# Kernel optimization log

Hardware: AMD Instinct MI355X
Metric: run time of the kernel (lower is better)

The kernel has to match this reference:

```python
import jax, jax.numpy as jnp
import numpy as np

D_MODEL = 1024
NUM_HEADS = 16
DEPTH = D_MODEL // NUM_HEADS
B, S = 2, 2048


def setup_inputs() -> dict:
    key = jax.random.key(0)
    ks = jax.random.split(key, 12)
    s = 1.0 / np.sqrt(D_MODEL)
    return {
        "query": jax.random.normal(ks[0], (B, S, D_MODEL), jnp.float32),
        "key": jax.random.normal(ks[1], (B, S, D_MODEL), jnp.float32),
        "value": jax.random.normal(ks[2], (B, S, D_MODEL), jnp.float32),
        "mask": jax.random.randint(ks[3], (B, S), 0, 2, jnp.int32),
        "Wq": jax.random.normal(ks[4], (D_MODEL, D_MODEL), jnp.float32) * s,
        "bq": jnp.zeros((D_MODEL,), jnp.float32),
        "Wk": jax.random.normal(ks[5], (D_MODEL, D_MODEL), jnp.float32) * s,
        "bk": jnp.zeros((D_MODEL,), jnp.float32),
        "Wv": jax.random.normal(ks[6], (D_MODEL, D_MODEL), jnp.float32) * s,
        "bv": jnp.zeros((D_MODEL,), jnp.float32),
        "Wo": jax.random.normal(ks[7], (D_MODEL, D_MODEL), jnp.float32) * s,
        "bo": jnp.zeros((D_MODEL,), jnp.float32),
    }


def _split_heads(x):
    # [B, S, D] -> [B, H, S, depth]
    b, s, _ = x.shape
    return x.reshape(b, s, NUM_HEADS, DEPTH).transpose(0, 2, 1, 3)


def reference(query, key, value, mask, Wq, bq, Wk, bk, Wv, bv, Wo, bo):
    q = _split_heads(query @ Wq.T + bq)
    k = _split_heads(key @ Wk.T + bk)
    v = _split_heads(value @ Wv.T + bv)
    scale = 1.0 / jnp.sqrt(jnp.float32(DEPTH))
    # [B, H, Sq, Sk]
    logits = jnp.einsum("bhqd,bhkd->bhqk", q, k) * scale
    logits = logits + mask.astype(logits.dtype)[:, None, None, :] * (-1e9)
    attn = jax.nn.softmax(logits, axis=-1)
    out = jnp.einsum("bhqk,bhkd->bhqd", attn, v)
    out = out.transpose(0, 2, 1, 3).reshape(query.shape[0], -1, D_MODEL)
    return out @ Wo.T + bo
```

## Files before the change

### kernel.cpp

```cpp
#include <hip/hip_runtime.h>

typedef _Float16 half8 __attribute__((ext_vector_type(8)));
typedef _Float16 half4 __attribute__((ext_vector_type(4)));
typedef __fp16  fp16x2 __attribute__((ext_vector_type(2)));
typedef float floatx4 __attribute__((ext_vector_type(4)));

#define D_MODEL 1024
#define NHEAD   16
#define DH      64
#define BATCH   2
#define SEQ     2048
#define M_TOT   4096
#define NT      (SEQ / 128)

#define SCALE_L2E 0.18033688011112042f
#define MASK_L2E  (-1.4426950408889634e9f)

#define GLD_LDS16(g, l)                                                          \
  __builtin_amdgcn_global_load_lds(                                              \
      (const __attribute__((address_space(1))) void*)(g),                        \
      (__attribute__((address_space(3))) void*)(l), 16, 0, 0)

__device__ inline half4 pk4(floatx4 v) {
  union { fp16x2 h2[2]; half4 h4; } u;
  u.h2[0] = __builtin_amdgcn_cvt_pkrtz(v[0], v[1]);
  u.h2[1] = __builtin_amdgcn_cvt_pkrtz(v[2], v[3]);
  return u.h4;
}

__global__ __launch_bounds__(256) void cvt_all(const float* __restrict__ q,
                                               const float* __restrict__ k,
                                               const float* __restrict__ v,
                                               const float* __restrict__ wq,
                                               const float* __restrict__ wk,
                                               const float* __restrict__ wv,
                                               const float* __restrict__ wo,
                                               _Float16* __restrict__ Xall,
                                               _Float16* __restrict__ Wall) {
  int bid = blockIdx.x;
  const float* src;
  _Float16* dst;
  if (bid < 6144) {
    int tsr = bid >> 11;
    src = (tsr == 0) ? q : (tsr == 1) ? k : v;
    dst = Xall + (size_t)tsr * 4194304;
    bid &= 2047;
  } else {
    int w = (bid - 6144) >> 9;
    src = (w == 0) ? wq : (w == 1) ? wk : (w == 2) ? wv : wo;
    dst = Wall + (size_t)w * 1048576;
    bid = (bid - 6144) & 511;
  }
  int off = bid * 2048 + threadIdx.x * 8;
  float4 a = *(const float4*)(src + off);
  float4 b = *(const float4*)(src + off + 4);
  half8 h;
  h[0] = (_Float16)a.x; h[1] = (_Float16)a.y; h[2] = (_Float16)a.z; h[3] = (_Float16)a.w;
  h[4] = (_Float16)b.x; h[5] = (_Float16)b.y; h[6] = (_Float16)b.z; h[7] = (_Float16)b.w;
  *(half8*)(dst + off) = h;
}

__global__ __launch_bounds__(256) void gemm_qkv(const _Float16* __restrict__ Xall,
                                                const _Float16* __restrict__ Wall,
                                                const float* __restrict__ bq,
                                                const float* __restrict__ bk,
                                                const float* __restrict__ bv,
                                                _Float16* __restrict__ Obase) {
  __shared__ alignas(16) char smem[32768];
  _Float16 (*As)[64]  = (_Float16(*)[64])smem;
  _Float16 (*Bs)[64]  = (_Float16(*)[64])(smem + 16384);
  _Float16 (*Ts)[136] = (_Float16(*)[136])smem;

  const int bid = blockIdx.x;
  const int xcd = bid & 7;
  const int g = bid >> 3;
  const int p = xcd * 12 + (g >> 3);
  const int z = p >> 5;
  const int m0 = (p & 31) * 128;
  const int n0 = (g & 7) * 128;

  const _Float16* X = Xall + (size_t)z * 4194304;
  const _Float16* W = Wall + (size_t)z * 1048576;
  const float* bias = (z == 0) ? bq : (z == 1) ? bk : bv;
  _Float16* out = Obase + (size_t)z * 4194304;

  const int t = threadIdx.x, lane = t & 63, wave = t >> 6;
  const int wr = wave >> 1, wc = wave & 1;
  const int fr = lane & 15, quad = lane >> 4, rg = quad * 4;
  const int fsw = fr & 7;

  floatx4 acc[4][4];
  for (int i = 0; i < 4; i++)
    for (int j = 0; j < 4; j++) acc[i][j] = (floatx4){0.f, 0.f, 0.f, 0.f};

  const int rl = lane >> 3, pc = lane & 7;
  const int gcol = ((pc ^ rl) * 8);
  const _Float16* gA[4];
  const _Float16* gB[4];
  _Float16* lA[4];
  _Float16* lB[4];
  for (int i = 0; i < 4; i++) {
    int row = wave * 32 + i * 8 + rl;
    gA[i] = X + (size_t)(m0 + row) * 1024 + gcol;
    gB[i] = W + (size_t)(n0 + row) * 1024 + gcol;
    lA[i] = &As[wave * 32 + i * 8][0];
    lB[i] = &Bs[wave * 32 + i * 8][0];
  }

  for (int k0 = 0; k0 < 1024; k0 += 64) {
    for (int i = 0; i < 4; i++) GLD_LDS16(gA[i] + k0, lA[i]);
    for (int i = 0; i < 4; i++) GLD_LDS16(gB[i] + k0, lB[i]);
    __syncthreads();

    for (int kk = 0; kk < 2; kk++) {
      const int csw = (((kk << 2) | quad) ^ fsw) * 8;
      half8 af[4], bw[4];
      for (int i = 0; i < 4; i++) {
        af[i] = *(const half8*)&As[wr * 64 + i * 16 + fr][csw];
        bw[i] = *(const half8*)&Bs[wc * 64 + i * 16 + fr][csw];
      }
      for (int i = 0; i < 4; i++)
        for (int j = 0; j < 4; j++)
          acc[i][j] = __builtin_amdgcn_mfma_f32_16x16x32_f16(af[i], bw[j], acc[i][j], 0, 0, 0);
    }
    __syncthreads();
  }

  if (z != 2) {
    for (int i = 0; i < 4; i++)
      for (int j = 0; j < 4; j++) {
        int n = n0 + wc * 64 + j * 16 + fr;
        float bv2 = bias[n];
        int hh = n >> 6, d = n & 63;
        for (int r = 0; r < 4; r++) {
          int m = m0 + wr * 64 + i * 16 + rg + r;
          int bb = m >> 11, s = m & 2047;
          out[(((size_t)(bb * NHEAD + hh)) * SEQ + s) * DH + d] =
              (_Float16)(acc[i][j][r] + bv2);
        }
      }
  } else {
    const int bb = m0 >> 11, s0 = m0 & 2047;
    for (int p2 = 0; p2 < 2; p2++) {
      __syncthreads();
      if (wc == p2) {
        for (int j = 0; j < 4; j++) {
          float bv2 = bias[n0 + p2 * 64 + j * 16 + fr];
          for (int i = 0; i < 4; i++)
            for (int r = 0; r < 4; r++)
              Ts[j * 16 + fr][wr * 64 + i * 16 + rg + r] =
                  (_Float16)(acc[i][j][r] + bv2);
        }
      }
      __syncthreads();
      int dd = t >> 2, c4 = (t & 3) * 32;
      int hh = (n0 >> 6) + p2;
      _Float16* dst = out + (((size_t)(bb * NHEAD + hh)) * DH + dd) * SEQ + s0;
      for (int u = 0; u < 4; u++)
        *(half8*)(dst + c4 + u * 8) = *(const half8*)&Ts[dd][c4 + u * 8];
    }
  }
}

__global__ __launch_bounds__(256) void gemm_wo(const _Float16* __restrict__ ctx,
                                               const _Float16* __restrict__ W,
                                               const float* __restrict__ bias,
                                               float* __restrict__ out) {
  __shared__ alignas(16) _Float16 As[128][64];
  __shared__ alignas(16) _Float16 Bs[128][64];

  const int t = threadIdx.x, lane = t & 63, wave = t >> 6;
  const int wr = wave >> 1, wc = wave & 1;
  const int m0 = blockIdx.y * 128, n0 = blockIdx.x * 128;
  const int fr = lane & 15, quad = lane >> 4, rg = quad * 4;
  const int fsw = fr & 7;

  floatx4 acc[4][4];
  for (int i = 0; i < 4; i++)
    for (int j = 0; j < 4; j++) acc[i][j] = (floatx4){0.f, 0.f, 0.f, 0.f};

  const int rl = lane >> 3, pc = lane & 7;
  const int gcol = ((pc ^ rl) * 8);
  const _Float16* gA[4];
  const _Float16* gB[4];
  _Float16* lA[4];
  _Float16* lB[4];
  for (int i = 0; i < 4; i++) {
    int row = wave * 32 + i * 8 + rl;
    gA[i] = ctx + (size_t)(m0 + row) * 1024 + gcol;
    gB[i] = W + (size_t)(n0 + row) * 1024 + gcol;
    lA[i] = &As[wave * 32 + i * 8][0];
    lB[i] = &Bs[wave * 32 + i * 8][0];
  }

  for (int k0 = 0; k0 < 1024; k0 += 64) {
    for (int i = 0; i < 4; i++) GLD_LDS16(gA[i] + k0, lA[i]);
    for (int i = 0; i < 4; i++) GLD_LDS16(gB[i] + k0, lB[i]);
    __syncthreads();

    for (int kk = 0; kk < 2; kk++) {
      const int csw = (((kk << 2) | quad) ^ fsw) * 8;
      half8 af[4], bw[4];
      for (int i = 0; i < 4; i++) {
        af[i] = *(const half8*)&As[wr * 64 + i * 16 + fr][csw];
        bw[i] = *(const half8*)&Bs[wc * 64 + i * 16 + fr][csw];
      }
      for (int i = 0; i < 4; i++)
        for (int j = 0; j < 4; j++)
          acc[i][j] = __builtin_amdgcn_mfma_f32_16x16x32_f16(af[i], bw[j], acc[i][j], 0, 0, 0);
    }
    __syncthreads();
  }

  for (int i = 0; i < 4; i++)
    for (int j = 0; j < 4; j++) {
      int n = n0 + wc * 64 + j * 16 + fr;
      float bv2 = bias[n];
      for (int r = 0; r < 4; r++) {
        int m = m0 + wr * 64 + i * 16 + rg + r;
        out[(size_t)m * D_MODEL + n] = acc[i][j][r] + bv2;
      }
    }
}

__global__ __launch_bounds__(256) void attn_kernel(const _Float16* __restrict__ Qp,
                                                   const _Float16* __restrict__ Kp,
                                                   const _Float16* __restrict__ VT,
                                                   const int* __restrict__ mask,
                                                   _Float16* __restrict__ ctx) {
  __shared__ alignas(16) _Float16 Ks[128][64];
  __shared__ alignas(16) _Float16 Vt[64][128];
  __shared__ float Msf[128];

  const int bid = blockIdx.x;
  const int hh = bid & 31;
  const int q0 = (bid >> 5) * 128;
  const int b = hh >> 4, h = hh & 15;

  const int t = threadIdx.x, lane = t & 63, wave = t >> 6;
  const int fr = lane & 15, quad = lane >> 4, fc = quad * 8;
  const int fsw = fr & 7;

  const _Float16* Kg  = Kp + (size_t)hh * SEQ * DH;
  const _Float16* VTg = VT + (size_t)hh * DH * SEQ;

  const _Float16* kG[4];
  {
    const int kr = lane >> 3, kp = lane & 7;
    for (int i = 0; i < 4; i++) {
      int krow = wave * 32 + i * 8 + kr;
      kG[i] = Kg + (size_t)krow * DH + ((kp ^ kr) * 8);
    }
  }

  const int svr = t >> 2;
  const int svc = (t & 3) * 4;

  half8 qf[2][2];
  {
    const _Float16* Qgw = Qp + ((size_t)hh * SEQ + q0 + wave * 32) * DH;
    for (int mi = 0; mi < 2; mi++)
      for (int kk = 0; kk < 2; kk++)
        qf[mi][kk] = *(const half8*)(Qgw + (mi * 16 + fr) * DH + kk * 32 + fc);
  }

  float lr[2][2] = {{0.f, 0.f}, {0.f, 0.f}};
  floatx4 oaccT[4][2];
  for (int dj = 0; dj < 4; dj++)
    for (int mi = 0; mi < 2; mi++) oaccT[dj][mi] = (floatx4){0.f, 0.f, 0.f, 0.f};

  for (int kt = 0; kt < NT; kt++) {
    const int k0 = kt * 128;

    for (int i = 0; i < 4; i++)
      GLD_LDS16(kG[i] + (size_t)k0 * DH, &Ks[wave * 32 + i * 8][0]);

    {
      const half8* gv = (const half8*)(VTg + (size_t)svr * SEQ + k0);
      half8 vb[4];
      for (int u = 0; u < 4; u++) vb[u] = gv[svc + u];
      const int rsw = svr & 7;
      for (int u = 0; u < 4; u++) {
        const int g = svc + u;
        const int t8p = g >> 2, par = (g >> 1) & 1, qA = (g & 1) * 2;
        const int v4lo = t8p * 8 + qA * 2 + par;
        const int v4hi = v4lo + 2;
        union { half8 h8; half4 h4[2]; } uv; uv.h8 = vb[u];
        *(half4*)&Vt[svr][((v4lo >> 1) ^ rsw) * 8 + (v4lo & 1) * 4] = uv.h4[0];
        *(half4*)&Vt[svr][((v4hi >> 1) ^ rsw) * 8 + (v4hi & 1) * 4] = uv.h4[1];
      }
    }
    if (t < 128) Msf[t] = (float)mask[b * SEQ + k0 + t] * MASK_L2E;
    __syncthreads();

    floatx4 saT[8][2];
#pragma unroll
    for (int t8 = 0; t8 < 8; t8++) {
      saT[t8][0] = (floatx4){0.f, 0.f, 0.f, 0.f};
      saT[t8][1] = (floatx4){0.f, 0.f, 0.f, 0.f};
      half8 kf0 = *(const half8*)&Ks[t8 * 16 + fr][(quad ^ fsw) * 8];
      half8 kf1 = *(const half8*)&Ks[t8 * 16 + fr][((4 | quad) ^ fsw) * 8];
      saT[t8][0] = __builtin_amdgcn_mfma_f32_16x16x32_f16(kf0, qf[0][0], saT[t8][0], 0, 0, 0);
      saT[t8][1] = __builtin_amdgcn_mfma_f32_16x16x32_f16(kf0, qf[1][0], saT[t8][1], 0, 0, 0);
      saT[t8][0] = __builtin_amdgcn_mfma_f32_16x16x32_f16(kf1, qf[0][1], saT[t8][0], 0, 0, 0);
      saT[t8][1] = __builtin_amdgcn_mfma_f32_16x16x32_f16(kf1, qf[1][1], saT[t8][1], 0, 0, 0);
    }

    floatx4 mk[8];
#pragma unroll
    for (int t8 = 0; t8 < 8; t8++)
      mk[t8] = *(const floatx4*)&Msf[t8 * 16 + quad * 4];

#pragma unroll
    for (int mi = 0; mi < 2; mi++) {
      float rs0 = 0.f, rs1 = 0.f;
#pragma unroll
      for (int t8 = 0; t8 < 8; t8++) {
        floatx4 p;
#pragma unroll
        for (int r = 0; r < 4; r++)
          p[r] = __builtin_amdgcn_exp2f(saT[t8][mi][r] * SCALE_L2E + mk[t8][r]);
        saT[t8][mi] = p;
        if (t8 & 1) rs1 += (p[0] + p[1]) + (p[2] + p[3]);
        else        rs0 += (p[0] + p[1]) + (p[2] + p[3]);
      }
      lr[mi][0] += rs0;
      lr[mi][1] += rs1;
    }

#pragma unroll
    for (int t8p = 0; t8p < 4; t8p++) {
      half4 pb0a = pk4(saT[2 * t8p][0]);
      half4 pb0b = pk4(saT[2 * t8p][1]);
      half4 pb1a = pk4(saT[2 * t8p + 1][0]);
      half4 pb1b = pk4(saT[2 * t8p + 1][1]);
      const int c = t8p * 4 + quad;
#pragma unroll
      for (int dj = 0; dj < 4; dj++) {
        const int d = dj * 16 + fr;
        union { half8 h8; half4 h4[2]; } uv;
        uv.h8 = *(const half8*)&Vt[d][(c ^ (d & 7)) * 8];
        oaccT[dj][0] = __builtin_amdgcn_mfma_f32_16x16x16f16(uv.h4[0], pb0a, oaccT[dj][0], 0, 0, 0);
        oaccT[dj][1] = __builtin_amdgcn_mfma_f32_16x16x16f16(uv.h4[0], pb0b, oaccT[dj][1], 0, 0, 0);
        oaccT[dj][0] = __builtin_amdgcn_mfma_f32_16x16x16f16(uv.h4[1], pb1a, oaccT[dj][0], 0, 0, 0);
        oaccT[dj][1] = __builtin_amdgcn_mfma_f32_16x16x16f16(uv.h4[1], pb1b, oaccT[dj][1], 0, 0, 0);
      }
    }
    __syncthreads();
  }

#pragma unroll
  for (int mi = 0; mi < 2; mi++) {
    float l = lr[mi][0] + lr[mi][1];
    l += __shfl_xor(l, 16);
    l += __shfl_xor(l, 32);
    float inv = 1.0f / l;
    int qrow = q0 + wave * 32 + mi * 16 + fr;
    _Float16* o = ctx + ((size_t)b * SEQ + qrow) * D_MODEL + h * DH;
#pragma unroll
    for (int dj = 0; dj < 4; dj++) {
      half4 st;
      for (int r = 0; r < 4; r++) st[r] = (_Float16)(oaccT[dj][mi][r] * inv);
      *(half4*)(o + dj * 16 + quad * 4) = st;
    }
  }
}

extern "C" void kernel_launch(void* const* d_in, const int* in_sizes, int n_in,
                              void* d_out, int out_size, void* d_ws, size_t ws_size,
                              hipStream_t stream) {
  const float* query = (const float*)d_in[0];
  const float* key   = (const float*)d_in[1];
  const float* value = (const float*)d_in[2];
  const int*   mask  = (const int*)d_in[3];
  const float* Wq = (const float*)d_in[4];
  const float* bq = (const float*)d_in[5];
  const float* Wk = (const float*)d_in[6];
  const float* bk = (const float*)d_in[7];
  const float* Wv = (const float*)d_in[8];
  const float* bv = (const float*)d_in[9];
  const float* Wo = (const float*)d_in[10];
  const float* bo = (const float*)d_in[11];

  char* ws = (char*)d_ws;
  _Float16* Xall = (_Float16*)(ws);
  _Float16* Wall = (_Float16*)(ws + (size_t)24 * 1024 * 1024);
  _Float16* Qp   = (_Float16*)(ws + (size_t)32 * 1024 * 1024);
  _Float16* ctx  = (_Float16*)(ws + (size_t)56 * 1024 * 1024);

  _Float16* Kp = Qp + (size_t)4194304;
  _Float16* VT = Qp + (size_t)8388608;

  cvt_all<<<8192, 256, 0, stream>>>(query, key, value, Wq, Wk, Wv, Wo, Xall, Wall);

  gemm_qkv<<<dim3(768), 256, 0, stream>>>(Xall, Wall, bq, bk, bv, Qp);

  attn_kernel<<<dim3(512), 256, 0, stream>>>(Qp, Kp, VT, mask, ctx);

  gemm_wo<<<dim3(8, 32), 256, 0, stream>>>(ctx, Wall + (size_t)3 * 1048576, bo, (float*)d_out);
}
```

Before: 238.8 us.

## Fuse fp32-to-fp16 activation conversion into the QKV projection GEMM

```diff
diff --git a/kernel.cpp b/kernel.cpp
--- a/kernel.cpp
+++ b/kernel.cpp
@@ -28,29 +28,16 @@
   return u.h4;
 }
 
-__global__ __launch_bounds__(256) void cvt_all(const float* __restrict__ q,
-                                               const float* __restrict__ k,
-                                               const float* __restrict__ v,
-                                               const float* __restrict__ wq,
-                                               const float* __restrict__ wk,
-                                               const float* __restrict__ wv,
-                                               const float* __restrict__ wo,
-                                               _Float16* __restrict__ Xall,
-                                               _Float16* __restrict__ Wall) {
+__global__ __launch_bounds__(256) void cvt_w(const float* __restrict__ wq,
+                                             const float* __restrict__ wk,
+                                             const float* __restrict__ wv,
+                                             const float* __restrict__ wo,
+                                             _Float16* __restrict__ Wall) {
   int bid = blockIdx.x;
-  const float* src;
-  _Float16* dst;
-  if (bid < 6144) {
-    int tsr = bid >> 11;
-    src = (tsr == 0) ? q : (tsr == 1) ? k : v;
-    dst = Xall + (size_t)tsr * 4194304;
-    bid &= 2047;
-  } else {
-    int w = (bid - 6144) >> 9;
-    src = (w == 0) ? wq : (w == 1) ? wk : (w == 2) ? wv : wo;
-    dst = Wall + (size_t)w * 1048576;
-    bid = (bid - 6144) & 511;
-  }
+  int w = bid >> 9;
+  const float* src = (w == 0) ? wq : (w == 1) ? wk : (w == 2) ? wv : wo;
+  _Float16* dst = Wall + (size_t)w * 1048576;
+  bid &= 511;
   int off = bid * 2048 + threadIdx.x * 8;
   float4 a = *(const float4*)(src + off);
   float4 b = *(const float4*)(src + off + 4);
@@ -60,16 +47,18 @@
   *(half8*)(dst + off) = h;
 }
 
-__global__ __launch_bounds__(256) void gemm_qkv(const _Float16* __restrict__ Xall,
+__global__ __launch_bounds__(256) void gemm_qkv(const float* __restrict__ query,
+                                                const float* __restrict__ key,
+                                                const float* __restrict__ value,
                                                 const _Float16* __restrict__ Wall,
                                                 const float* __restrict__ bq,
                                                 const float* __restrict__ bk,
                                                 const float* __restrict__ bv,
                                                 _Float16* __restrict__ Obase) {
-  __shared__ alignas(16) char smem[32768];
-  _Float16 (*As)[64]  = (_Float16(*)[64])smem;
-  _Float16 (*Bs)[64]  = (_Float16(*)[64])(smem + 16384);
-  _Float16 (*Ts)[136] = (_Float16(*)[136])smem;
+  __shared__ alignas(16) char smem[49152];
+  float    (*As32)[64] = (float(*)[64])smem;
+  _Float16 (*Bs)[64]   = (_Float16(*)[64])(smem + 32768);
+  _Float16 (*Ts)[136]  = (_Float16(*)[136])smem;
 
   const int bid = blockIdx.x;
   const int xcd = bid & 7;
@@ -79,7 +68,7 @@
   const int m0 = (p & 31) * 128;
   const int n0 = (g & 7) * 128;
 
-  const _Float16* X = Xall + (size_t)z * 4194304;
+  const float* X = (z == 0) ? query : (z == 1) ? key : value;
   const _Float16* W = Wall + (size_t)z * 1048576;
   const float* bias = (z == 0) ? bq : (z == 1) ? bk : bv;
   _Float16* out = Obase + (size_t)z * 4194304;
@@ -93,31 +82,44 @@
   for (int i = 0; i < 4; i++)
     for (int j = 0; j < 4; j++) acc[i][j] = (floatx4){0.f, 0.f, 0.f, 0.f};
 
+  const int rl4 = lane >> 4, pc16 = lane & 15;
+  const int u32l = pc16 >> 1, hh16 = pc16 & 1;
+  const float* gA[8];
+  float* lA[8];
+  for (int i = 0; i < 8; i++) {
+    int row = wave * 32 + i * 4 + rl4;
+    gA[i] = X + (size_t)(m0 + row) * 1024 + ((u32l ^ (row & 7)) * 8 + hh16 * 4);
+    lA[i] = &As32[wave * 32 + i * 4][0];
+  }
   const int rl = lane >> 3, pc = lane & 7;
-  const int gcol = ((pc ^ rl) * 8);
-  const _Float16* gA[4];
+  const int gcolB = ((pc ^ rl) * 8);
   const _Float16* gB[4];
-  _Float16* lA[4];
   _Float16* lB[4];
   for (int i = 0; i < 4; i++) {
     int row = wave * 32 + i * 8 + rl;
-    gA[i] = X + (size_t)(m0 + row) * 1024 + gcol;
-    gB[i] = W + (size_t)(n0 + row) * 1024 + gcol;
-    lA[i] = &As[wave * 32 + i * 8][0];
+    gB[i] = W + (size_t)(n0 + row) * 1024 + gcolB;
     lB[i] = &Bs[wave * 32 + i * 8][0];
   }
 
   for (int k0 = 0; k0 < 1024; k0 += 64) {
-    for (int i = 0; i < 4; i++) GLD_LDS16(gA[i] + k0, lA[i]);
+    for (int i = 0; i < 8; i++) GLD_LDS16(gA[i] + k0, lA[i]);
     for (int i = 0; i < 4; i++) GLD_LDS16(gB[i] + k0, lB[i]);
     __syncthreads();
 
     for (int kk = 0; kk < 2; kk++) {
-      const int csw = (((kk << 2) | quad) ^ fsw) * 8;
+      const int u = ((kk << 2) | quad) ^ fsw;
       half8 af[4], bw[4];
       for (int i = 0; i < 4; i++) {
-        af[i] = *(const half8*)&As[wr * 64 + i * 16 + fr][csw];
-        bw[i] = *(const half8*)&Bs[wc * 64 + i * 16 + fr][csw];
+        const float* ar = &As32[wr * 64 + i * 16 + fr][u * 8];
+        floatx4 a0 = *(const floatx4*)ar;
+        floatx4 a1 = *(const floatx4*)(ar + 4);
+        union { fp16x2 h2[4]; half8 h8; } ua;
+        ua.h2[0] = __builtin_amdgcn_cvt_pkrtz(a0[0], a0[1]);
+        ua.h2[1] = __builtin_amdgcn_cvt_pkrtz(a0[2], a0[3]);
+        ua.h2[2] = __builtin_amdgcn_cvt_pkrtz(a1[0], a1[1]);
+        ua.h2[3] = __builtin_amdgcn_cvt_pkrtz(a1[2], a1[3]);
+        af[i] = ua.h8;
+        bw[i] = *(const half8*)&Bs[wc * 64 + i * 16 + fr][u * 8];
       }
       for (int i = 0; i < 4; i++)
         for (int j = 0; j < 4; j++)
@@ -156,8 +158,8 @@
       int dd = t >> 2, c4 = (t & 3) * 32;
       int hh = (n0 >> 6) + p2;
       _Float16* dst = out + (((size_t)(bb * NHEAD + hh)) * DH + dd) * SEQ + s0;
-      for (int u = 0; u < 4; u++)
-        *(half8*)(dst + c4 + u * 8) = *(const half8*)&Ts[dd][c4 + u * 8];
+      for (int u2 = 0; u2 < 4; u2++)
+        *(half8*)(dst + c4 + u2 * 8) = *(const half8*)&Ts[dd][c4 + u2 * 8];
     }
   }
 }
@@ -383,7 +385,6 @@
   const float* bo = (const float*)d_in[11];
 
   char* ws = (char*)d_ws;
-  _Float16* Xall = (_Float16*)(ws);
   _Float16* Wall = (_Float16*)(ws + (size_t)24 * 1024 * 1024);
   _Float16* Qp   = (_Float16*)(ws + (size_t)32 * 1024 * 1024);
   _Float16* ctx  = (_Float16*)(ws + (size_t)56 * 1024 * 1024);
@@ -391,9 +392,9 @@
   _Float16* Kp = Qp + (size_t)4194304;
   _Float16* VT = Qp + (size_t)8388608;
 
-  cvt_all<<<8192, 256, 0, stream>>>(query, key, value, Wq, Wk, Wv, Wo, Xall, Wall);
-
-  gemm_qkv<<<dim3(768), 256, 0, stream>>>(Xall, Wall, bq, bk, bv, Qp);
+  cvt_w<<<2048, 256, 0, stream>>>(Wq, Wk, Wv, Wo, Wall);
+
+  gemm_qkv<<<dim3(768), 256, 0, stream>>>(query, key, value, Wall, bq, bk, bv, Qp);
 
   attn_kernel<<<dim3(512), 256, 0, stream>>>(Qp, Kp, VT, mask, ctx);
 
```

Result: no change. 242.8 us (+1.7%).
